# Kernel tuning notes

Hardware: AMD Instinct MI355X
Metric: run time of the kernel (lower is better)

The kernel has to match this reference:

```python
import jax, jax.numpy as jnp
import numpy as np

B, N, D, E, H = 128, 64, 128, 32, 256

def setup_inputs() -> dict:
    key = jax.random.key(0)
    ks = jax.random.split(key, 6)
    nodes = jax.random.normal(ks[0], (B, N, D), dtype=jnp.float32)
    edges = jax.random.normal(ks[1], (B, N * N, E), dtype=jnp.float32)
    W1 = jax.random.normal(ks[2], (2 * D + E, H), dtype=jnp.float32) * (1.0 / np.sqrt(2 * D + E))
    b1 = jnp.zeros((H,), dtype=jnp.float32)
    W2 = jax.random.normal(ks[3], (H, H), dtype=jnp.float32) * (1.0 / np.sqrt(H))
    b2 = jnp.zeros((H,), dtype=jnp.float32)
    W3 = jax.random.normal(ks[4], (H, 1), dtype=jnp.float32) * (1.0 / np.sqrt(H))
    b3 = jnp.zeros((1,), dtype=jnp.float32)
    return {"nodes": nodes, "edges": edges, "W1": W1, "b1": b1, "W2": W2, "b2": b2, "W3": W3, "b3": b3}

def reference(nodes, edges, W1, b1, W2, b2, W3, b3):
    b, n, d = nodes.shape
    # state_i[p] = nodes[p // n] (each node repeated n times consecutively)
    state_i = jnp.broadcast_to(nodes[:, :, None, :], (b, n, n, d)).reshape(b, n * n, d)
    # state_j[p] = nodes[p % n] (whole node list tiled n times)
    state_j = jnp.broadcast_to(nodes[:, None, :, :], (b, n, n, d)).reshape(b, n * n, d)
    concat = jnp.concatenate([state_i, edges, state_j], axis=-1)  # [b, n*n, 2d+e]
    a1 = jax.nn.relu(jnp.einsum('bpf,fh->bph', concat, W1) + b1)
    a2 = jax.nn.relu(jnp.einsum('bph,hk->bpk', a1, W2) + b2)
    return jnp.einsum('bph,ho->bpo', a2, W3) + b3  # [b, n*n, 1]
```

## Files before the change

### kernel.cpp

```cpp
#include <hip/hip_runtime.h>
#include <hip/hip_bf16.h>

typedef __bf16 bf16_t;
typedef __bf16 bf16x8 __attribute__((ext_vector_type(8)));
typedef float  f32x4  __attribute__((ext_vector_type(4)));

static __device__ __forceinline__ f32x4 mfma16(bf16x8 a, bf16x8 b, f32x4 c) {
    return __builtin_amdgcn_mfma_f32_16x16x32_bf16(a, b, c, 0, 0, 0);
}

__global__ void prep_pack(const float* __restrict__ W1, const float* __restrict__ W2,
                          bf16_t* __restrict__ W1ef, bf16_t* __restrict__ W2f) {
    int t = blockIdx.x * blockDim.x + threadIdx.x;
    int l = t & 63, g = l >> 4, c = l & 15;
    if (t < 1024) {
        int ht = t >> 6;
        int hcol = 32 * (ht >> 1) + 8 * (c >> 2) + 4 * (ht & 1) + (c & 3);
        #pragma unroll
        for (int j = 0; j < 8; ++j)
            W1ef[t * 8 + j] = (bf16_t)W1[(128 + 8 * g + j) * 256 + hcol];
    } else if (t < 1024 + 8192) {
        int t2 = t - 1024;
        int ks = t2 >> 10;
        int ct = (t2 >> 6) & 15;
        #pragma unroll
        for (int j = 0; j < 8; ++j) {
            int krow = 32 * ks + 8 * g + 4 * (j >> 2) + (j & 3);
            W2f[t2 * 8 + j] = (bf16_t)W2[krow * 256 + ct * 16 + c];
        }
    }
}

__global__ __launch_bounds__(256) void prep_pij(const float* __restrict__ nodes,
                                                const float* __restrict__ W1,
                                                const float* __restrict__ b1,
                                                float* __restrict__ Pi,
                                                bf16_t* __restrict__ Pjb) {
    int b = blockIdx.x >> 2;
    int q = blockIdx.x & 3;
    int h = threadIdx.x;
    const float* nb = nodes + (b * 64 + q * 16) * 128;
    float ai[16], aj[16];
    float bias = b1[h];
    #pragma unroll
    for (int ii = 0; ii < 16; ++ii) { ai[ii] = bias; aj[ii] = 0.f; }
    for (int d = 0; d < 128; ++d) {
        float wi = W1[d * 256 + h];
        float wj = W1[(160 + d) * 256 + h];
        #pragma unroll
        for (int ii = 0; ii < 16; ++ii) {
            float s = nb[ii * 128 + d];
            ai[ii] = fmaf(s, wi, ai[ii]);
            aj[ii] = fmaf(s, wj, aj[ii]);
        }
    }
    #pragma unroll
    for (int ii = 0; ii < 16; ++ii) {
        Pi[(b * 64 + q * 16 + ii) * 256 + h] = ai[ii];
        Pjb[(b * 64 + q * 16 + ii) * 256 + h] = (bf16_t)aj[ii];
    }
}

__global__ __launch_bounds__(512, 2) void mlp_main(
    const float* __restrict__ edges,
    const float* __restrict__ Pi, const bf16_t* __restrict__ Pjb,
    const bf16_t* __restrict__ W1ef, const bf16_t* __restrict__ W2f,
    const float* __restrict__ b2, const float* __restrict__ W3,
    const float* __restrict__ b3, float* __restrict__ out) {

    __shared__ bf16_t a1f[2][16384];
    __shared__ bf16_t elds[2][2048];
    __shared__ float part[2][4][64];

    const int p = blockIdx.x;
    const int xb = (p & 7) * 64 + (p >> 3);
    const int tid = threadIdx.x;
    const int w = tid >> 6, l = tid & 63, g = l >> 4, c = l & 15;
    const int rw = w & 3;
    const int b = xb >> 2;
    const f32x4 z4 = {0.f, 0.f, 0.f, 0.f};
    const float bias3 = b3[0];
    const long outbase = (long)xb * 1024;

    if (w < 4) {
        bf16x8 wf[4];
        #pragma unroll
        for (int q = 0; q < 4; ++q)
            wf[q] = *(const bf16x8*)&W1ef[((4 * rw + q) * 64 + l) * 8];

        bf16x8 pjb[4][2];
        #pragma unroll
        for (int pt = 0; pt < 4; ++pt)
            #pragma unroll
            for (int o = 0; o < 2; ++o)
                pjb[pt][o] = *(const bf16x8*)&Pjb[((long)(b * 64 + 16 * pt + c)) * 256
                                                  + 32 * (2 * rw + o) + 8 * g];

        const int sg = (tid >> 4) & 3, sc = tid & 15;
        const long erowbase = (long)xb * 1024 + 16 * rw + sc;

        f32x4 es0, es1;
        {
            const float* ep = edges + erowbase * 32 + 8 * sg;
            es0 = *(const f32x4*)ep; es1 = *(const f32x4*)(ep + 4);
            bf16x8 ev;
            #pragma unroll
            for (int j = 0; j < 4; ++j) { ev[j] = (bf16_t)es0[j]; ev[4 + j] = (bf16_t)es1[j]; }
            *(bf16x8*)&elds[0][tid * 8] = ev;
        }
        __syncthreads();

        for (int t = 0; t < 17; ++t) {
            const int cur = t & 1;
            if (t < 16) {
                if (t < 15) {
                    const float* ep = edges + (erowbase + 64 * (t + 1)) * 32 + 8 * sg;
                    es0 = *(const f32x4*)ep; es1 = *(const f32x4*)(ep + 4);
                }
                const float* PiB = Pi + ((long)xb * 16 + t) * 256;
                f32x4 piv[2][2];
                #pragma unroll
                for (int o = 0; o < 2; ++o) {
                    const float* pp = PiB + 32 * (2 * rw + o) + 8 * g;
                    piv[o][0] = *(const f32x4*)pp;
                    piv[o][1] = *(const f32x4*)(pp + 4);
                }
                bf16x8 ebf[4];
                #pragma unroll
                for (int pt = 0; pt < 4; ++pt)
                    ebf[pt] = *(const bf16x8*)&elds[cur][(pt * 64 + l) * 8];
                #pragma unroll
                for (int pt = 0; pt < 4; ++pt) {
                    #pragma unroll
                    for (int o = 0; o < 2; ++o) {
                        bf16x8 oct;
                        #pragma unroll
                        for (int z = 0; z < 2; ++z) {
                            f32x4 a = mfma16(wf[2 * o + z], ebf[pt], z4);
                            #pragma unroll
                            for (int r = 0; r < 4; ++r) {
                                float v = a[r] + piv[o][z][r] + (float)pjb[pt][o][4 * z + r];
                                v = v > 0.f ? v : 0.f;
                                oct[4 * z + r] = (bf16_t)v;
                            }
                        }
                        *(bf16x8*)&a1f[cur][((pt * 8 + 2 * rw + o) * 64 + l) * 8] = oct;
                    }
                }
                if (t < 15) {
                    bf16x8 ev;
                    #pragma unroll
                    for (int j = 0; j < 4; ++j) { ev[j] = (bf16_t)es0[j]; ev[4 + j] = (bf16_t)es1[j]; }
                    *(bf16x8*)&elds[cur ^ 1][tid * 8] = ev;
                }
            }
            if (t >= 2 && tid < 64) {
                float s = bias3;
                #pragma unroll
                for (int cw = 0; cw < 4; ++cw) s += part[cur][cw][tid];
                out[outbase + (t - 2) * 64 + tid] = s;
            }
            __syncthreads();
        }
        if (tid < 64) {
            float s = bias3;
            #pragma unroll
            for (int cw = 0; cw < 4; ++cw) s += part[1][cw][tid];
            out[outbase + 15 * 64 + tid] = s;
        }
    } else {
        __syncthreads();

        for (int t = 0; t < 17; ++t) {
            if (t >= 1) {
                const int buf = (t - 1) & 1;
                f32x4 acc2[4][4];
                #pragma unroll
                for (int pt = 0; pt < 4; ++pt)
                    #pragma unroll
                    for (int cc = 0; cc < 4; ++cc) acc2[pt][cc] = z4;
                #pragma unroll
                for (int ks = 0; ks < 8; ++ks) {
                    bf16x8 af[4];
                    #pragma unroll
                    for (int pt = 0; pt < 4; ++pt)
                        af[pt] = *(const bf16x8*)&a1f[buf][((pt * 8 + ks) * 64 + l) * 8];
                    #pragma unroll
                    for (int cc = 0; cc < 4; ++cc) {
                        bf16x8 w2 = *(const bf16x8*)&W2f[((ks * 16 + 4 * rw + cc) * 64 + l) * 8];
                        #pragma unroll
                        for (int pt = 0; pt < 4; ++pt)
                            acc2[pt][cc] = mfma16(w2, af[pt], acc2[pt][cc]);
                    }
                }
                #pragma unroll
                for (int pt = 0; pt < 4; ++pt) {
                    float s = 0.f;
                    #pragma unroll
                    for (int cc = 0; cc < 4; ++cc) {
                        f32x4 b2q = *(const f32x4*)&b2[64 * rw + 16 * cc + 4 * g];
                        f32x4 w3q = *(const f32x4*)&W3[64 * rw + 16 * cc + 4 * g];
                        #pragma unroll
                        for (int r = 0; r < 4; ++r) {
                            float v = acc2[pt][cc][r] + b2q[r];
                            v = v > 0.f ? v : 0.f;
                            s = fmaf(v, w3q[r], s);
                        }
                    }
                    s += __shfl_xor(s, 16);
                    s += __shfl_xor(s, 32);
                    if (g == 0) part[buf][rw][pt * 16 + c] = s;
                }
            }
            __syncthreads();
        }
    }
}

extern "C" void kernel_launch(void* const* d_in, const int* in_sizes, int n_in,
                              void* d_out, int out_size, void* d_ws, size_t ws_size,
                              hipStream_t stream) {
    const float* nodes = (const float*)d_in[0];
    const float* edges = (const float*)d_in[1];
    const float* W1    = (const float*)d_in[2];
    const float* b1    = (const float*)d_in[3];
    const float* W2    = (const float*)d_in[4];
    const float* b2    = (const float*)d_in[5];
    const float* W3    = (const float*)d_in[6];
    const float* b3    = (const float*)d_in[7];
    float* out = (float*)d_out;

    char* ws = (char*)d_ws;
    float*  Pi   = (float*)ws;
    bf16_t* Pjb  = (bf16_t*)(ws + (size_t)8 * 1024 * 1024);
    bf16_t* W2f  = (bf16_t*)(ws + (size_t)12 * 1024 * 1024);
    bf16_t* W1ef = (bf16_t*)(ws + (size_t)12 * 1024 * 1024 + 131072);

    prep_pack<<<dim3(36), dim3(256), 0, stream>>>(W1, W2, W1ef, W2f);
    prep_pij<<<dim3(512), dim3(256), 0, stream>>>(nodes, W1, b1, Pi, Pjb);
    mlp_main<<<dim3(512), dim3(512), 0, stream>>>(edges, Pi, Pjb, W1ef, W2f, b2, W3, b3, out);
}
```

Baseline: 122.4 us.

## Merge producer/consumer warp groups into unified 4-wave pipeline; split prep_pij finer

```diff
diff --git a/kernel.cpp b/kernel.cpp
--- a/kernel.cpp
+++ b/kernel.cpp
@@ -36,32 +36,32 @@
                                                 const float* __restrict__ b1,
                                                 float* __restrict__ Pi,
                                                 bf16_t* __restrict__ Pjb) {
-    int b = blockIdx.x >> 2;
-    int q = blockIdx.x & 3;
+    int b = blockIdx.x >> 3;
+    int q = blockIdx.x & 7;
     int h = threadIdx.x;
-    const float* nb = nodes + (b * 64 + q * 16) * 128;
-    float ai[16], aj[16];
+    const float* nb = nodes + (b * 64 + q * 8) * 128;
+    float ai[8], aj[8];
     float bias = b1[h];
     #pragma unroll
-    for (int ii = 0; ii < 16; ++ii) { ai[ii] = bias; aj[ii] = 0.f; }
+    for (int ii = 0; ii < 8; ++ii) { ai[ii] = bias; aj[ii] = 0.f; }
     for (int d = 0; d < 128; ++d) {
         float wi = W1[d * 256 + h];
         float wj = W1[(160 + d) * 256 + h];
         #pragma unroll
-        for (int ii = 0; ii < 16; ++ii) {
+        for (int ii = 0; ii < 8; ++ii) {
             float s = nb[ii * 128 + d];
             ai[ii] = fmaf(s, wi, ai[ii]);
             aj[ii] = fmaf(s, wj, aj[ii]);
         }
     }
     #pragma unroll
-    for (int ii = 0; ii < 16; ++ii) {
-        Pi[(b * 64 + q * 16 + ii) * 256 + h] = ai[ii];
-        Pjb[(b * 64 + q * 16 + ii) * 256 + h] = (bf16_t)aj[ii];
-    }
-}
-
-__global__ __launch_bounds__(512, 2) void mlp_main(
+    for (int ii = 0; ii < 8; ++ii) {
+        Pi[(b * 64 + q * 8 + ii) * 256 + h] = ai[ii];
+        Pjb[(b * 64 + q * 8 + ii) * 256 + h] = (bf16_t)aj[ii];
+    }
+}
+
+__global__ __launch_bounds__(256, 2) void mlp_main(
     const float* __restrict__ edges,
     const float* __restrict__ Pi, const bf16_t* __restrict__ Pjb,
     const bf16_t* __restrict__ W1ef, const bf16_t* __restrict__ W2f,
@@ -76,144 +76,134 @@
     const int xb = (p & 7) * 64 + (p >> 3);
     const int tid = threadIdx.x;
     const int w = tid >> 6, l = tid & 63, g = l >> 4, c = l & 15;
-    const int rw = w & 3;
     const int b = xb >> 2;
     const f32x4 z4 = {0.f, 0.f, 0.f, 0.f};
     const float bias3 = b3[0];
     const long outbase = (long)xb * 1024;
 
-    if (w < 4) {
-        bf16x8 wf[4];
-        #pragma unroll
-        for (int q = 0; q < 4; ++q)
-            wf[q] = *(const bf16x8*)&W1ef[((4 * rw + q) * 64 + l) * 8];
-
-        bf16x8 pjb[4][2];
-        #pragma unroll
-        for (int pt = 0; pt < 4; ++pt)
-            #pragma unroll
-            for (int o = 0; o < 2; ++o)
-                pjb[pt][o] = *(const bf16x8*)&Pjb[((long)(b * 64 + 16 * pt + c)) * 256
-                                                  + 32 * (2 * rw + o) + 8 * g];
-
-        const int sg = (tid >> 4) & 3, sc = tid & 15;
-        const long erowbase = (long)xb * 1024 + 16 * rw + sc;
-
-        f32x4 es0, es1;
+    const int sg = (tid >> 4) & 3, sc = tid & 15;
+    const long erowbase = (long)xb * 1024 + 16 * w + sc;
+
+    f32x4 es0, es1;
+    {
+        const float* ep = edges + erowbase * 32 + 8 * sg;
+        es0 = *(const f32x4*)ep; es1 = *(const f32x4*)(ep + 4);
+        bf16x8 ev;
+        #pragma unroll
+        for (int j = 0; j < 4; ++j) { ev[j] = (bf16_t)es0[j]; ev[4 + j] = (bf16_t)es1[j]; }
+        *(bf16x8*)&elds[0][tid * 8] = ev;
+    }
+    __syncthreads();
+
+    for (int t = 0; t < 16; ++t) {
+        const int cur = t & 1;
+
+        if (t < 15) {
+            const float* ep = edges + (erowbase + 64 * (t + 1)) * 32 + 8 * sg;
+            es0 = *(const f32x4*)ep; es1 = *(const f32x4*)(ep + 4);
+        }
+
         {
-            const float* ep = edges + erowbase * 32 + 8 * sg;
-            es0 = *(const f32x4*)ep; es1 = *(const f32x4*)(ep + 4);
+            bf16x8 wf[4];
+            #pragma unroll
+            for (int q = 0; q < 4; ++q)
+                wf[q] = *(const bf16x8*)&W1ef[((4 * w + q) * 64 + l) * 8];
+            const float* PiB = Pi + ((long)xb * 16 + t) * 256;
+            f32x4 piv[2][2];
+            #pragma unroll
+            for (int o = 0; o < 2; ++o) {
+                const float* pp = PiB + 32 * (2 * w + o) + 8 * g;
+                piv[o][0] = *(const f32x4*)pp;
+                piv[o][1] = *(const f32x4*)(pp + 4);
+            }
+            bf16x8 ebf[4];
+            #pragma unroll
+            for (int pt = 0; pt < 4; ++pt)
+                ebf[pt] = *(const bf16x8*)&elds[cur][(pt * 64 + l) * 8];
+            #pragma unroll
+            for (int pt = 0; pt < 4; ++pt) {
+                #pragma unroll
+                for (int o = 0; o < 2; ++o) {
+                    bf16x8 pj = *(const bf16x8*)&Pjb[((long)(b * 64 + 16 * pt + c)) * 256
+                                                     + 32 * (2 * w + o) + 8 * g];
+                    bf16x8 oct;
+                    #pragma unroll
+                    for (int z = 0; z < 2; ++z) {
+                        f32x4 a = mfma16(wf[2 * o + z], ebf[pt], z4);
+                        #pragma unroll
+                        for (int r = 0; r < 4; ++r) {
+                            float v = a[r] + piv[o][z][r] + (float)pj[4 * z + r];
+                            v = v > 0.f ? v : 0.f;
+                            oct[4 * z + r] = (bf16_t)v;
+                        }
+                    }
+                    *(bf16x8*)&a1f[cur][((pt * 8 + 2 * w + o) * 64 + l) * 8] = oct;
+                }
+            }
+        }
+
+        if (t < 15) {
             bf16x8 ev;
             #pragma unroll
             for (int j = 0; j < 4; ++j) { ev[j] = (bf16_t)es0[j]; ev[4 + j] = (bf16_t)es1[j]; }
-            *(bf16x8*)&elds[0][tid * 8] = ev;
+            *(bf16x8*)&elds[cur ^ 1][tid * 8] = ev;
         }
         __syncthreads();
 
-        for (int t = 0; t < 17; ++t) {
-            const int cur = t & 1;
-            if (t < 16) {
-                if (t < 15) {
-                    const float* ep = edges + (erowbase + 64 * (t + 1)) * 32 + 8 * sg;
-                    es0 = *(const f32x4*)ep; es1 = *(const f32x4*)(ep + 4);
+        if (t > 0 && tid < 64) {
+            float s = bias3;
+            #pragma unroll
+            for (int cw = 0; cw < 4; ++cw) s += part[cur ^ 1][cw][tid];
+            out[outbase + (t - 1) * 64 + tid] = s;
+        }
+
+        {
+            f32x4 acc2[4][4];
+            #pragma unroll
+            for (int pt = 0; pt < 4; ++pt)
+                #pragma unroll
+                for (int cc = 0; cc < 4; ++cc) acc2[pt][cc] = z4;
+            #pragma unroll
+            for (int ks = 0; ks < 8; ++ks) {
+                bf16x8 af[4];
+                #pragma unroll
+                for (int pt = 0; pt < 4; ++pt)
+                    af[pt] = *(const bf16x8*)&a1f[cur][((pt * 8 + ks) * 64 + l) * 8];
+                #pragma unroll
+                for (int cc = 0; cc < 4; ++cc) {
+                    bf16x8 w2 = *(const bf16x8*)&W2f[((ks * 16 + 4 * w + cc) * 64 + l) * 8];
+                    #pragma unroll
+                    for (int pt = 0; pt < 4; ++pt)
+                        acc2[pt][cc] = mfma16(w2, af[pt], acc2[pt][cc]);
                 }
-                const float* PiB = Pi + ((long)xb * 16 + t) * 256;
-                f32x4 piv[2][2];
-                #pragma unroll
-                for (int o = 0; o < 2; ++o) {
-                    const float* pp = PiB + 32 * (2 * rw + o) + 8 * g;
-                    piv[o][0] = *(const f32x4*)pp;
-                    piv[o][1] = *(const f32x4*)(pp + 4);
-                }
-                bf16x8 ebf[4];
-                #pragma unroll
-                for (int pt = 0; pt < 4; ++pt)
-                    ebf[pt] = *(const bf16x8*)&elds[cur][(pt * 64 + l) * 8];
-                #pragma unroll
-                for (int pt = 0; pt < 4; ++pt) {
+            }
+            #pragma unroll
+            for (int pt = 0; pt < 4; ++pt) {
+                float s = 0.f;
+                #pragma unroll
+                for (int cc = 0; cc < 4; ++cc) {
+                    f32x4 b2q = *(const f32x4*)&b2[64 * w + 16 * cc + 4 * g];
+                    f32x4 w3q = *(const f32x4*)&W3[64 * w + 16 * cc + 4 * g];
                     #pragma unroll
-                    for (int o = 0; o < 2; ++o) {
-                        bf16x8 oct;
-                        #pragma unroll
-                        for (int z = 0; z < 2; ++z) {
-                            f32x4 a = mfma16(wf[2 * o + z], ebf[pt], z4);
-                            #pragma unroll
-                            for (int r = 0; r < 4; ++r) {
-                                float v = a[r] + piv[o][z][r] + (float)pjb[pt][o][4 * z + r];
-                                v = v > 0.f ? v : 0.f;
-                                oct[4 * z + r] = (bf16_t)v;
-                            }
-                        }
-                        *(bf16x8*)&a1f[cur][((pt * 8 + 2 * rw + o) * 64 + l) * 8] = oct;
+                    for (int r = 0; r < 4; ++r) {
+                        float v = acc2[pt][cc][r] + b2q[r];
+                        v = v > 0.f ? v : 0.f;
+                        s = fmaf(v, w3q[r], s);
                     }
                 }
-                if (t < 15) {
-                    bf16x8 ev;
-                    #pragma unroll
-                    for (int j = 0; j < 4; ++j) { ev[j] = (bf16_t)es0[j]; ev[4 + j] = (bf16_t)es1[j]; }
-                    *(bf16x8*)&elds[cur ^ 1][tid * 8] = ev;
-                }
-            }
-            if (t >= 2 && tid < 64) {
-                float s = bias3;
-                #pragma unroll
-                for (int cw = 0; cw < 4; ++cw) s += part[cur][cw][tid];
-                out[outbase + (t - 2) * 64 + tid] = s;
-            }
-            __syncthreads();
-        }
-        if (tid < 64) {
-            float s = bias3;
-            #pragma unroll
-            for (int cw = 0; cw < 4; ++cw) s += part[1][cw][tid];
-            out[outbase + 15 * 64 + tid] = s;
-        }
-    } else {
-        __syncthreads();
-
-        for (int t = 0; t < 17; ++t) {
-            if (t >= 1) {
-                const int buf = (t - 1) & 1;
-                f32x4 acc2[4][4];
-                #pragma unroll
-                for (int pt = 0; pt < 4; ++pt)
-                    #pragma unroll
-                    for (int cc = 0; cc < 4; ++cc) acc2[pt][cc] = z4;
-                #pragma unroll
-                for (int ks = 0; ks < 8; ++ks) {
-                    bf16x8 af[4];
-                    #pragma unroll
-                    for (int pt = 0; pt < 4; ++pt)
-                        af[pt] = *(const bf16x8*)&a1f[buf][((pt * 8 + ks) * 64 + l) * 8];
-                    #pragma unroll
-                    for (int cc = 0; cc < 4; ++cc) {
-                        bf16x8 w2 = *(const bf16x8*)&W2f[((ks * 16 + 4 * rw + cc) * 64 + l) * 8];
-                        #pragma unroll
-                        for (int pt = 0; pt < 4; ++pt)
-                            acc2[pt][cc] = mfma16(w2, af[pt], acc2[pt][cc]);
-                    }
-                }
-                #pragma unroll
-                for (int pt = 0; pt < 4; ++pt) {
-                    float s = 0.f;
-                    #pragma unroll
-                    for (int cc = 0; cc < 4; ++cc) {
-                        f32x4 b2q = *(const f32x4*)&b2[64 * rw + 16 * cc + 4 * g];
-                        f32x4 w3q = *(const f32x4*)&W3[64 * rw + 16 * cc + 4 * g];
-                        #pragma unroll
-                        for (int r = 0; r < 4; ++r) {
-                            float v = acc2[pt][cc][r] + b2q[r];
-                            v = v > 0.f ? v : 0.f;
-                            s = fmaf(v, w3q[r], s);
-                        }
-                    }
-                    s += __shfl_xor(s, 16);
-                    s += __shfl_xor(s, 32);
-                    if (g == 0) part[buf][rw][pt * 16 + c] = s;
-                }
-            }
-            __syncthreads();
-        }
+                s += __shfl_xor(s, 16);
+                s += __shfl_xor(s, 32);
+                if (g == 0) part[cur][w][pt * 16 + c] = s;
+            }
+        }
+    }
+
+    __syncthreads();
+    if (tid < 64) {
+        float s = bias3;
+        #pragma unroll
+        for (int cw = 0; cw < 4; ++cw) s += part[1][cw][tid];
+        out[outbase + 15 * 64 + tid] = s;
     }
 }
 
@@ -237,6 +227,6 @@
     bf16_t* W1ef = (bf16_t*)(ws + (size_t)12 * 1024 * 1024 + 131072);
 
     prep_pack<<<dim3(36), dim3(256), 0, stream>>>(W1, W2, W1ef, W2f);
-    prep_pij<<<dim3(512), dim3(256), 0, stream>>>(nodes, W1, b1, Pi, Pjb);
-    mlp_main<<<dim3(512), dim3(512), 0, stream>>>(edges, Pi, Pjb, W1ef, W2f, b2, W3, b3, out);
-}
+    prep_pij<<<dim3(1024), dim3(256), 0, stream>>>(nodes, W1, b1, Pi, Pjb);
+    mlp_main<<<dim3(512), dim3(256), 0, stream>>>(edges, Pi, Pjb, W1ef, W2f, b2, W3, b3, out);
+}
```

Measured after the change: 243.1 us. 98.7% more time.
